# Optimization experiments

Measured on AMD Instinct MI355X. Metric: run time of the kernel, lower is better.

## Reference

```python
import jax, jax.numpy as jnp
import numpy as np


def gcn_conv(h, edge_index, num_nodes):
    # Symmetric-normalized GCN aggregation: out[i] = sum_{(j->i)} h[j] / sqrt(deg(i)*deg(j))
    row, col = edge_index[0], edge_index[1]
    deg = jax.ops.segment_sum(jnp.ones(col.shape, dtype=h.dtype), col, num_segments=num_nodes)
    d_inv_sqrt = jnp.where(deg > 0, jax.lax.rsqrt(jnp.maximum(deg, 1.0)), 0.0)
    w = d_inv_sqrt[row] * d_inv_sqrt[col]           # [E]
    msg = h[row] * w[:, None]                        # [E, D] gather + scale
    return jax.ops.segment_sum(msg, col, num_segments=num_nodes)  # [N, D] scatter-add


def setup_inputs() -> dict:
    key = jax.random.key(0)
    k1, k2, k3, k4 = jax.random.split(key, 4)
    N, E, F_IN, F_HID, F_OUT = 100000, 1600000, 128, 64, 40
    x = jax.random.normal(k1, (N, F_IN), dtype=jnp.float32)
    edge_index = jax.random.randint(k2, (2, E), 0, N, dtype=jnp.int64)
    # xavier_uniform with gain=1.414 (as in reset_parameters); biases zero
    def xavier(k, shape, gain=1.414):
        fan_out, fan_in = shape
        a = gain * np.sqrt(6.0 / (fan_in + fan_out))
        return jax.random.uniform(k, shape, jnp.float32, -a, a)
    W1 = xavier(k3, (F_HID, F_IN))
    b1 = jnp.zeros((F_HID,), dtype=jnp.float32)
    W2 = xavier(k4, (F_OUT, F_HID))
    b2 = jnp.zeros((F_OUT,), dtype=jnp.float32)
    return {"x": x, "edge_index": edge_index, "W1": W1, "b1": b1, "W2": W2, "b2": b2}


def reference(x, edge_index, W1, b1, W2, b2):
    # GNN.forward with num_layers=2, use_mp=True, eval mode (dropout inactive)
    N = x.shape[0]
    h = x @ W1.T                      # [N, nhid]
    h = gcn_conv(h, edge_index, N)
    h = jax.nn.relu(h + b1)
    h = h @ W2.T                      # [N, nclass]
    h = gcn_conv(h, edge_index, N)
    return h + b2
```

## Files before the change

### kernel.cpp

```cpp
#include <hip/hip_runtime.h>
#include <hip/hip_fp16.h>


typedef __attribute__((ext_vector_type(8))) _Float16 half8v;
typedef __attribute__((ext_vector_type(4))) float   float4v;

__global__ void k_detect(const int* __restrict__ ed, int* __restrict__ flag, int nwords) {
  __shared__ int any;
  if (threadIdx.x == 0) any = 0;
  __syncthreads();
  #pragma unroll
  for (int u = 0; u < 8; ++u) {
    int idx = 2 * (threadIdx.x * 8 + u) + 1;
    if (idx < nwords && ed[idx] != 0) any = 1;
  }
  __syncthreads();
  if (threadIdx.x == 0) *flag = any ? 0 : 1;
}

__global__ void k_binfill(const int* __restrict__ ed, const int* __restrict__ flag,
                          int* __restrict__ gbincnt, unsigned* __restrict__ binbuf,
                          int E, int cap) {
  __shared__ int hist[512];
  __shared__ int cursor[512];
  __shared__ unsigned rec[4096];
  __shared__ unsigned short binv[4096];
  int t = threadIdx.x;
  hist[t] = 0; hist[t + 256] = 0;
  __syncthreads();
  const int is64 = *flag;
  const int base = blockIdx.x * 4096;
  const int nE = min(4096, E - base);
  for (int j = t; j < nE; j += 256) {
    int e = base + j;
    int r = is64 ? ed[2 * e] : ed[e];
    int c = is64 ? ed[2 * (E + e)] : ed[E + e];
    rec[j] = (unsigned)r | ((unsigned)(c & 255) << 17);
    binv[j] = (unsigned short)(c >> 8);
    atomicAdd(&hist[c >> 8], 1);
  }
  __syncthreads();
  for (int b = t; b < 512; b += 256) {
    int h = hist[b];
    cursor[b] = h ? atomicAdd(&gbincnt[b], h) : 0;
  }
  __syncthreads();
  for (int j = t; j < nE; j += 256) {
    int bin = binv[j];
    int pos = atomicAdd(&cursor[bin], 1);
    if (pos < cap)
      binbuf[(size_t)bin * cap + pos] = rec[j];
  }
}

__global__ void k_binscan(const int* __restrict__ gbincnt, int* __restrict__ gbase,
                          int* __restrict__ rowptr, int NBINS, int N, int cap) {
  __shared__ int sd[512];
  int t = threadIdx.x;
  #pragma unroll
  for (int u = 0; u < 2; ++u) {
    int i = t + 256 * u;
    sd[i] = (i < NBINS) ? min(gbincnt[i], cap) : 0;
  }
  __syncthreads();
  for (int off = 1; off < 512; off <<= 1) {
    int v0 = (t >= off) ? sd[t - off] : 0;
    int i1 = t + 256;
    int v1 = sd[i1 - off];
    __syncthreads();
    sd[t] += v0; sd[i1] += v1;
    __syncthreads();
  }
  #pragma unroll
  for (int u = 0; u < 2; ++u) {
    int i = t + 256 * u;
    if (i < NBINS) gbase[i] = (i == 0) ? 0 : sd[i - 1];
  }
  if (t == 0) rowptr[N] = sd[NBINS - 1];
}

__global__ void k_degscat(const unsigned* __restrict__ binbuf, const int* __restrict__ gbincnt,
                          const int* __restrict__ gbase, float* __restrict__ dis,
                          int* __restrict__ rowptr, int* __restrict__ srcs, int N, int cap) {
  __shared__ int cnt[256];
  __shared__ int sd[256];
  __shared__ int cursor[256];
  __shared__ unsigned rec[8192];
  int t = threadIdx.x, b = blockIdx.x;
  cnt[t] = 0;
  __syncthreads();
  int n = min(gbincnt[b], cap);
  const unsigned* buf = binbuf + (size_t)b * cap;
  for (int j = t; j < n; j += 256) {
    unsigned v = buf[j];
    rec[j] = v;
    atomicAdd(&cnt[v >> 17], 1);
  }
  __syncthreads();
  sd[t] = cnt[t];
  __syncthreads();
  for (int off = 1; off < 256; off <<= 1) {
    int v = (t >= off) ? sd[t - off] : 0;
    __syncthreads();
    sd[t] += v;
    __syncthreads();
  }
  int rp = gbase[b] + ((t == 0) ? 0 : sd[t - 1]);
  cursor[t] = rp;
  int node = b * 256 + t;
  if (node < N) {
    int d = cnt[t];
    dis[node] = (d > 0) ? rsqrtf((float)d) : 0.f;
    rowptr[node] = rp;
  }
  __syncthreads();
  for (int j = t; j < n; j += 256) {
    unsigned v = rec[j];
    int pos = atomicAdd(&cursor[v >> 17], 1);
    srcs[pos] = (int)(v & 0x1FFFF);
  }
}

__launch_bounds__(256)
__global__ void k_gemm1_mfma(const float* __restrict__ X, const float* __restrict__ W,
                             const float* __restrict__ dis, __half* __restrict__ Y, int N) {
  __shared__ _Float16 xl[128 * 128];
  __shared__ _Float16 wl[64 * 128];
  const int t = threadIdx.x;
  const int row0 = blockIdx.x * 128;

  {
    int n = t >> 2, kb = (t & 3) * 32;
    const float* src = W + n * 128 + kb;
    #pragma unroll
    for (int j = 0; j < 4; ++j) {
      float4 va = *(const float4*)&src[j * 8];
      float4 vb = *(const float4*)&src[j * 8 + 4];
      _Float16 h8[8] = {(_Float16)va.x, (_Float16)va.y, (_Float16)va.z, (_Float16)va.w,
                        (_Float16)vb.x, (_Float16)vb.y, (_Float16)vb.z, (_Float16)vb.w};
      int k = kb + j * 8;
      *(float4*)&wl[n * 128 + (k ^ ((n & 7) * 8))] = *(float4*)h8;
    }
  }
  {
    int r = t >> 1, kb = (t & 1) * 64;
    int row = row0 + r;
    #pragma unroll
    for (int j = 0; j < 8; ++j) {
      float4 va = make_float4(0.f, 0.f, 0.f, 0.f), vb = va;
      if (row < N) {
        va = *(const float4*)&X[(size_t)row * 128 + kb + j * 8];
        vb = *(const float4*)&X[(size_t)row * 128 + kb + j * 8 + 4];
      }
      _Float16 h8[8] = {(_Float16)va.x, (_Float16)va.y, (_Float16)va.z, (_Float16)va.w,
                        (_Float16)vb.x, (_Float16)vb.y, (_Float16)vb.z, (_Float16)vb.w};
      int k = kb + j * 8;
      *(float4*)&xl[r * 128 + (k ^ ((r & 7) * 8))] = *(float4*)h8;
    }
  }
  __syncthreads();

  const int w = t >> 6, l = t & 63;
  const int m0 = w * 32;
  const int lr = l & 15, q = l >> 4;

  float4v acc[2][4] = {};
  #pragma unroll
  for (int kc = 0; kc < 4; ++kc) {
    half8v a[2], b[4];
    #pragma unroll
    for (int mt = 0; mt < 2; ++mt) {
      int m = m0 + mt * 16 + lr;
      int k = (kc * 32 + q * 8) ^ ((m & 7) * 8);
      a[mt] = *(half8v*)&xl[m * 128 + k];
    }
    #pragma unroll
    for (int nt = 0; nt < 4; ++nt) {
      int n = nt * 16 + lr;
      int k = (kc * 32 + q * 8) ^ ((n & 7) * 8);
      b[nt] = *(half8v*)&wl[n * 128 + k];
    }
    #pragma unroll
    for (int mt = 0; mt < 2; ++mt)
      #pragma unroll
      for (int nt = 0; nt < 4; ++nt)
        acc[mt][nt] = __builtin_amdgcn_mfma_f32_16x16x32_f16(a[mt], b[nt], acc[mt][nt], 0, 0, 0);
  }

  #pragma unroll
  for (int mt = 0; mt < 2; ++mt) {
    #pragma unroll
    for (int r = 0; r < 4; ++r) {
      int row = row0 + m0 + mt * 16 + q * 4 + r;
      if (row < N) {
        float dr = dis[row];
        #pragma unroll
        for (int nt = 0; nt < 4; ++nt)
          Y[(size_t)row * 64 + nt * 16 + lr] = __float2half_rn(acc[mt][nt][r] * dr);
      }
    }
  }
}

__launch_bounds__(256)
__global__ void k_gemm2_mfma(const __half* __restrict__ Xh, const float* __restrict__ W,
                             const float* __restrict__ dis, __half* __restrict__ Y, int N) {
  __shared__ _Float16 xl[128 * 64];
  __shared__ _Float16 wl[48 * 64];
  const int t = threadIdx.x;
  const int row0 = blockIdx.x * 128;

  for (int i = t; i < 48 * 8; i += 256) {
    int c = i >> 3, kq = i & 7;
    _Float16 h8[8];
    #pragma unroll
    for (int j = 0; j < 8; ++j)
      h8[j] = (c < 40) ? (_Float16)W[c * 64 + kq * 8 + j] : (_Float16)0.f;
    *(float4*)&wl[c * 64 + ((kq * 8) ^ ((c & 7) * 8))] = *(float4*)h8;
  }
  for (int i = t; i < 1024; i += 256) {
    int r = i >> 3, kq = i & 7;
    int row = row0 + r;
    float4 v = make_float4(0.f, 0.f, 0.f, 0.f);
    if (row < N) v = *(const float4*)&Xh[(size_t)row * 64 + kq * 8];
    *(float4*)&xl[r * 64 + ((kq * 8) ^ ((r & 7) * 8))] = v;
  }
  __syncthreads();

  const int w = t >> 6, l = t & 63;
  const int m0 = w * 32;
  const int lr = l & 15, q = l >> 4;

  float4v acc[2][3] = {};
  #pragma unroll
  for (int kc = 0; kc < 2; ++kc) {
    half8v a[2], b[3];
    #pragma unroll
    for (int mt = 0; mt < 2; ++mt) {
      int m = m0 + mt * 16 + lr;
      int k = (kc * 32 + q * 8) ^ ((m & 7) * 8);
      a[mt] = *(half8v*)&xl[m * 64 + k];
    }
    #pragma unroll
    for (int nt = 0; nt < 3; ++nt) {
      int n = nt * 16 + lr;
      int k = (kc * 32 + q * 8) ^ ((n & 7) * 8);
      b[nt] = *(half8v*)&wl[n * 64 + k];
    }
    #pragma unroll
    for (int mt = 0; mt < 2; ++mt)
      #pragma unroll
      for (int nt = 0; nt < 3; ++nt)
        acc[mt][nt] = __builtin_amdgcn_mfma_f32_16x16x32_f16(a[mt], b[nt], acc[mt][nt], 0, 0, 0);
  }

  #pragma unroll
  for (int mt = 0; mt < 2; ++mt) {
    #pragma unroll
    for (int r = 0; r < 4; ++r) {
      int row = row0 + m0 + mt * 16 + q * 4 + r;
      if (row < N) {
        float dr = dis[row];
        #pragma unroll
        for (int nt = 0; nt < 3; ++nt) {
          int col = nt * 16 + lr;
          if (col < 40)
            Y[(size_t)row * 40 + col] = __float2half_rn(acc[mt][nt][r] * dr);
        }
      }
    }
  }
}

__launch_bounds__(256)
__global__ void k_conv64(const __half* __restrict__ H, const int* __restrict__ rowptr,
                         const int* __restrict__ srcs, const float* __restrict__ dis,
                         const float* __restrict__ b1, __half* __restrict__ out, int N) {
  int node = blockIdx.x * 4 + (threadIdx.x >> 6);
  if (node >= N) return;
  int lane = threadIdx.x & 63;
  int g = lane >> 3, li = lane & 7;
  int s = rowptr[node], e = rowptr[node + 1];
  int last = e - 1;
  float a0 = 0.f, a1 = 0.f, a2 = 0.f, a3 = 0.f,
        a4 = 0.f, a5 = 0.f, a6 = 0.f, a7 = 0.f;
  for (int p = s; p < e; p += 32) {
    int sv = srcs[min(p + (lane & 31), last)];
    #pragma unroll
    for (int u = 0; u < 4; ++u) {
      int src = __shfl(sv, 8 * u + g);
      float4 raw = *(const float4*)&H[(size_t)src * 64 + 8 * li];
      if (p + 8 * u + g < e) {
        const __half2* hp = (const __half2*)&raw;
        float2 f0 = __half22float2(hp[0]);
        float2 f1 = __half22float2(hp[1]);
        float2 f2 = __half22float2(hp[2]);
        float2 f3 = __half22float2(hp[3]);
        a0 += f0.x; a1 += f0.y; a2 += f1.x; a3 += f1.y;
        a4 += f2.x; a5 += f2.y; a6 += f3.x; a7 += f3.y;
      }
    }
  }
  #pragma unroll
  for (int off = 8; off <= 32; off <<= 1) {
    a0 += __shfl_xor(a0, off); a1 += __shfl_xor(a1, off);
    a2 += __shfl_xor(a2, off); a3 += __shfl_xor(a3, off);
    a4 += __shfl_xor(a4, off); a5 += __shfl_xor(a5, off);
    a6 += __shfl_xor(a6, off); a7 += __shfl_xor(a7, off);
  }
  if (g == 0) {
    float dn = dis[node];
    const float* bb = b1 + 8 * li;
    __half hv[8];
    hv[0] = __float2half_rn(fmaxf(fmaf(a0, dn, bb[0]), 0.f));
    hv[1] = __float2half_rn(fmaxf(fmaf(a1, dn, bb[1]), 0.f));
    hv[2] = __float2half_rn(fmaxf(fmaf(a2, dn, bb[2]), 0.f));
    hv[3] = __float2half_rn(fmaxf(fmaf(a3, dn, bb[3]), 0.f));
    hv[4] = __float2half_rn(fmaxf(fmaf(a4, dn, bb[4]), 0.f));
    hv[5] = __float2half_rn(fmaxf(fmaf(a5, dn, bb[5]), 0.f));
    hv[6] = __float2half_rn(fmaxf(fmaf(a6, dn, bb[6]), 0.f));
    hv[7] = __float2half_rn(fmaxf(fmaf(a7, dn, bb[7]), 0.f));
    *(float4*)&out[(size_t)node * 64 + 8 * li] = *(float4*)hv;
  }
}

__launch_bounds__(256)
__global__ void k_conv40(const __half* __restrict__ H, const int* __restrict__ rowptr,
                         const int* __restrict__ srcs, const float* __restrict__ dis,
                         const float* __restrict__ b2, float* __restrict__ out, int N) {
  int node = blockIdx.x * 4 + (threadIdx.x >> 6);
  if (node >= N) return;
  int lane = threadIdx.x & 63;
  int g = lane >> 3, li = lane & 7;
  bool act = li < 5;
  int s = rowptr[node], e = rowptr[node + 1];
  int last = e - 1;
  float a0 = 0.f, a1 = 0.f, a2 = 0.f, a3 = 0.f,
        a4 = 0.f, a5 = 0.f, a6 = 0.f, a7 = 0.f;
  for (int p = s; p < e; p += 32) {
    int sv = srcs[min(p + (lane & 31), last)];
    #pragma unroll
    for (int u = 0; u < 4; ++u) {
      int src = __shfl(sv, 8 * u + g);
      if (act) {
        float4 raw = *(const float4*)&H[(size_t)src * 40 + 8 * li];
        if (p + 8 * u + g < e) {
          const __half2* hp = (const __half2*)&raw;
          float2 f0 = __half22float2(hp[0]);
          float2 f1 = __half22float2(hp[1]);
          float2 f2 = __half22float2(hp[2]);
          float2 f3 = __half22float2(hp[3]);
          a0 += f0.x; a1 += f0.y; a2 += f1.x; a3 += f1.y;
          a4 += f2.x; a5 += f2.y; a6 += f3.x; a7 += f3.y;
        }
      }
    }
  }
  #pragma unroll
  for (int off = 8; off <= 32; off <<= 1) {
    a0 += __shfl_xor(a0, off); a1 += __shfl_xor(a1, off);
    a2 += __shfl_xor(a2, off); a3 += __shfl_xor(a3, off);
    a4 += __shfl_xor(a4, off); a5 += __shfl_xor(a5, off);
    a6 += __shfl_xor(a6, off); a7 += __shfl_xor(a7, off);
  }
  if (g == 0 && act) {
    float dn = dis[node];
    const float* bb = b2 + 8 * li;
    float4 v0 = make_float4(fmaf(a0, dn, bb[0]), fmaf(a1, dn, bb[1]),
                            fmaf(a2, dn, bb[2]), fmaf(a3, dn, bb[3]));
    float4 v1 = make_float4(fmaf(a4, dn, bb[4]), fmaf(a5, dn, bb[5]),
                            fmaf(a6, dn, bb[6]), fmaf(a7, dn, bb[7]));
    *(float4*)&out[(size_t)node * 40 + 8 * li] = v0;
    *(float4*)&out[(size_t)node * 40 + 8 * li + 4] = v1;
  }
}

extern "C" void kernel_launch(void* const* d_in, const int* in_sizes, int n_in,
                              void* d_out, int out_size, void* d_ws, size_t ws_size,
                              hipStream_t stream) {
  const float* x  = (const float*)d_in[0];
  const int*   ed = (const int*)d_in[1];
  const float* W1 = (const float*)d_in[2];
  const float* b1 = (const float*)d_in[3];
  const float* W2 = (const float*)d_in[4];
  const float* b2 = (const float*)d_in[5];
  float* out = (float*)d_out;

  const int FIN = 128, FH = 64, FO = 40;
  const int N = in_sizes[0] / FIN;
  const int E = in_sizes[1] / 2;
  const int NBINS = (N + 255) >> 8;

  char* ws = (char*)d_ws;
  size_t off = 0;
  auto alloc = [&](size_t bytes) {
    void* p = ws + off;
    off = (off + bytes + 255) & ~(size_t)255;
    return p;
  };
  int*    flag    = (int*)alloc(4);
  int*    gbincnt = (int*)alloc(512 * 4);
  int*    gbase   = (int*)alloc(512 * 4);
  float*  dis     = (float*)alloc((size_t)N * 4);
  int*    rowptr  = (int*)alloc(((size_t)N + 1) * 4);
  int*    srcs    = (int*)alloc((size_t)E * 4);
  __half* h1      = (__half*)alloc((size_t)N * FH * 2);
  __half* h1b     = (__half*)alloc((size_t)N * FH * 2);
  __half* h2      = (__half*)alloc((size_t)N * FO * 2);
  int cap = (int)(((size_t)N * FH * 2) / ((size_t)NBINS * 4));
  if (cap > 8192) cap = 8192;
  unsigned* binbuf = (unsigned*)h1;

  hipMemsetAsync(gbincnt, 0, 512 * 4, stream);
  k_detect<<<1, 256, 0, stream>>>(ed, flag, in_sizes[1]);

  int fb = (E + 4095) / 4096;
  k_binfill<<<fb, 256, 0, stream>>>(ed, flag, gbincnt, binbuf, E, cap);
  k_binscan<<<1, 256, 0, stream>>>(gbincnt, gbase, rowptr, NBINS, N, cap);
  k_degscat<<<NBINS, 256, 0, stream>>>(binbuf, gbincnt, gbase, dis, rowptr, srcs, N, cap);

  int mb = (N + 127) / 128;
  int cb = (N + 3) / 4;
  k_gemm1_mfma<<<mb, 256, 0, stream>>>(x, W1, dis, h1, N);
  k_conv64<<<cb, 256, 0, stream>>>(h1, rowptr, srcs, dis, b1, h1b, N);
  k_gemm2_mfma<<<mb, 256, 0, stream>>>(h1b, W2, dis, h2, N);
  k_conv40<<<cb, 256, 0, stream>>>(h2, rowptr, srcs, dis, b2, out, N);
}
```

Baseline: 251.5 us.

## Quantize layer-2 features to int8, fold detect and scan kernels, recoalesce GEMM loads

Layer-2 features are now quantized to int8 with one fp32 scale per row, in 64-byte rows, so the second aggregation gathers fewer bytes per edge. The k_detect kernel is folded into every k_binfill block, and the k_binscan prefix scan is recomputed redundantly in every k_degscat block, which removes two launches. The gemm1 staging loads are reorganized so consecutive threads read consecutive float4s. The int8 quantization loses accuracy compared with fp16 and may fail tolerance checks.

```diff
diff --git a/kernel.cpp b/kernel.cpp
--- a/kernel.cpp
+++ b/kernel.cpp
@@ -5,30 +5,29 @@
 typedef __attribute__((ext_vector_type(8))) _Float16 half8v;
 typedef __attribute__((ext_vector_type(4))) float   float4v;
 
-__global__ void k_detect(const int* __restrict__ ed, int* __restrict__ flag, int nwords) {
-  __shared__ int any;
-  if (threadIdx.x == 0) any = 0;
-  __syncthreads();
-  #pragma unroll
-  for (int u = 0; u < 8; ++u) {
-    int idx = 2 * (threadIdx.x * 8 + u) + 1;
-    if (idx < nwords && ed[idx] != 0) any = 1;
-  }
-  __syncthreads();
-  if (threadIdx.x == 0) *flag = any ? 0 : 1;
-}
-
-__global__ void k_binfill(const int* __restrict__ ed, const int* __restrict__ flag,
+__global__ void k_binfill(const int* __restrict__ ed,
                           int* __restrict__ gbincnt, unsigned* __restrict__ binbuf,
                           int E, int cap) {
   __shared__ int hist[512];
   __shared__ int cursor[512];
   __shared__ unsigned rec[4096];
   __shared__ unsigned short binv[4096];
+  __shared__ int s_is64;
   int t = threadIdx.x;
   hist[t] = 0; hist[t + 256] = 0;
-  __syncthreads();
-  const int is64 = *flag;
+  if (t == 0) s_is64 = 1;
+  __syncthreads();
+  {
+    int any = 0;
+    #pragma unroll
+    for (int u = 0; u < 8; ++u) {
+      int idx = 2 * (t * 8 + u) + 1;
+      if (idx < 2 * E && ed[idx] != 0) any = 1;
+    }
+    if (any) s_is64 = 0;
+  }
+  __syncthreads();
+  const int is64 = s_is64;
   const int base = blockIdx.x * 4096;
   const int nE = min(4096, E - base);
   for (int j = t; j < nE; j += 256) {
@@ -53,42 +52,29 @@
   }
 }
 
-__global__ void k_binscan(const int* __restrict__ gbincnt, int* __restrict__ gbase,
-                          int* __restrict__ rowptr, int NBINS, int N, int cap) {
+__global__ void k_degscat(const unsigned* __restrict__ binbuf, const int* __restrict__ gbincnt,
+                          float* __restrict__ dis, int* __restrict__ rowptr,
+                          int* __restrict__ srcs, int NBINS, int N, int cap) {
   __shared__ int sd[512];
-  int t = threadIdx.x;
-  #pragma unroll
-  for (int u = 0; u < 2; ++u) {
-    int i = t + 256 * u;
-    sd[i] = (i < NBINS) ? min(gbincnt[i], cap) : 0;
-  }
-  __syncthreads();
-  for (int off = 1; off < 512; off <<= 1) {
-    int v0 = (t >= off) ? sd[t - off] : 0;
-    int i1 = t + 256;
-    int v1 = sd[i1 - off];
-    __syncthreads();
-    sd[t] += v0; sd[i1] += v1;
-    __syncthreads();
-  }
-  #pragma unroll
-  for (int u = 0; u < 2; ++u) {
-    int i = t + 256 * u;
-    if (i < NBINS) gbase[i] = (i == 0) ? 0 : sd[i - 1];
-  }
-  if (t == 0) rowptr[N] = sd[NBINS - 1];
-}
-
-__global__ void k_degscat(const unsigned* __restrict__ binbuf, const int* __restrict__ gbincnt,
-                          const int* __restrict__ gbase, float* __restrict__ dis,
-                          int* __restrict__ rowptr, int* __restrict__ srcs, int N, int cap) {
   __shared__ int cnt[256];
-  __shared__ int sd[256];
+  __shared__ int sc[256];
   __shared__ int cursor[256];
   __shared__ unsigned rec[8192];
   int t = threadIdx.x, b = blockIdx.x;
+  sd[t]       = (t < NBINS)       ? min(gbincnt[t], cap)       : 0;
+  sd[t + 256] = (t + 256 < NBINS) ? min(gbincnt[t + 256], cap) : 0;
   cnt[t] = 0;
   __syncthreads();
+  for (int off = 1; off < 512; off <<= 1) {
+    int v0 = (t >= off) ? sd[t - off] : 0;
+    int v1 = sd[t + 256 - off];
+    __syncthreads();
+    sd[t] += v0; sd[t + 256] += v1;
+    __syncthreads();
+  }
+  const int mybase = (b == 0) ? 0 : sd[b - 1];
+  if (b == NBINS - 1 && t == 0) rowptr[N] = sd[NBINS - 1];
+
   int n = min(gbincnt[b], cap);
   const unsigned* buf = binbuf + (size_t)b * cap;
   for (int j = t; j < n; j += 256) {
@@ -97,15 +83,15 @@
     atomicAdd(&cnt[v >> 17], 1);
   }
   __syncthreads();
-  sd[t] = cnt[t];
+  sc[t] = cnt[t];
   __syncthreads();
   for (int off = 1; off < 256; off <<= 1) {
-    int v = (t >= off) ? sd[t - off] : 0;
+    int v = (t >= off) ? sc[t - off] : 0;
     __syncthreads();
-    sd[t] += v;
+    sc[t] += v;
     __syncthreads();
   }
-  int rp = gbase[b] + ((t == 0) ? 0 : sd[t - 1]);
+  int rp = mybase + ((t == 0) ? 0 : sc[t - 1]);
   cursor[t] = rp;
   int node = b * 256 + t;
   if (node < N) {
@@ -129,34 +115,25 @@
   const int t = threadIdx.x;
   const int row0 = blockIdx.x * 128;
 
-  {
-    int n = t >> 2, kb = (t & 3) * 32;
-    const float* src = W + n * 128 + kb;
-    #pragma unroll
-    for (int j = 0; j < 4; ++j) {
-      float4 va = *(const float4*)&src[j * 8];
-      float4 vb = *(const float4*)&src[j * 8 + 4];
-      _Float16 h8[8] = {(_Float16)va.x, (_Float16)va.y, (_Float16)va.z, (_Float16)va.w,
-                        (_Float16)vb.x, (_Float16)vb.y, (_Float16)vb.z, (_Float16)vb.w};
-      int k = kb + j * 8;
-      *(float4*)&wl[n * 128 + (k ^ ((n & 7) * 8))] = *(float4*)h8;
-    }
-  }
-  {
-    int r = t >> 1, kb = (t & 1) * 64;
+  #pragma unroll
+  for (int j = 0; j < 8; ++j) {
+    int qq = t + 256 * j;
+    int r = qq >> 5, k4 = qq & 31;
+    float4 v = *(const float4*)&W[(size_t)r * 128 + k4 * 4];
+    _Float16 h4[4] = {(_Float16)v.x, (_Float16)v.y, (_Float16)v.z, (_Float16)v.w};
+    int k = (k4 * 4) ^ ((r & 7) * 8);
+    *(float2*)&wl[r * 128 + k] = *(float2*)h4;
+  }
+  #pragma unroll
+  for (int j = 0; j < 16; ++j) {
+    int qq = t + 256 * j;
+    int r = qq >> 5, k4 = qq & 31;
     int row = row0 + r;
-    #pragma unroll
-    for (int j = 0; j < 8; ++j) {
-      float4 va = make_float4(0.f, 0.f, 0.f, 0.f), vb = va;
-      if (row < N) {
-        va = *(const float4*)&X[(size_t)row * 128 + kb + j * 8];
-        vb = *(const float4*)&X[(size_t)row * 128 + kb + j * 8 + 4];
-      }
-      _Float16 h8[8] = {(_Float16)va.x, (_Float16)va.y, (_Float16)va.z, (_Float16)va.w,
-                        (_Float16)vb.x, (_Float16)vb.y, (_Float16)vb.z, (_Float16)vb.w};
-      int k = kb + j * 8;
-      *(float4*)&xl[r * 128 + (k ^ ((r & 7) * 8))] = *(float4*)h8;
-    }
+    float4 v = make_float4(0.f, 0.f, 0.f, 0.f);
+    if (row < N) v = *(const float4*)&X[(size_t)row * 128 + k4 * 4];
+    _Float16 h4[4] = {(_Float16)v.x, (_Float16)v.y, (_Float16)v.z, (_Float16)v.w};
+    int k = (k4 * 4) ^ ((r & 7) * 8);
+    *(float2*)&xl[r * 128 + k] = *(float2*)h4;
   }
   __syncthreads();
 
@@ -204,7 +181,8 @@
 
 __launch_bounds__(256)
 __global__ void k_gemm2_mfma(const __half* __restrict__ Xh, const float* __restrict__ W,
-                             const float* __restrict__ dis, __half* __restrict__ Y, int N) {
+                             const float* __restrict__ dis, unsigned char* __restrict__ h2,
+                             int N) {
   __shared__ _Float16 xl[128 * 64];
   __shared__ _Float16 wl[48 * 64];
   const int t = threadIdx.x;
@@ -261,12 +239,27 @@
       int row = row0 + m0 + mt * 16 + q * 4 + r;
       if (row < N) {
         float dr = dis[row];
+        float v0 = acc[mt][0][r] * dr;
+        float v1 = acc[mt][1][r] * dr;
+        float v2 = acc[mt][2][r] * dr;
+        float m = fmaxf(fabsf(v0), fmaxf(fabsf(v1), fabsf(v2)));
         #pragma unroll
-        for (int nt = 0; nt < 3; ++nt) {
-          int col = nt * 16 + lr;
-          if (col < 40)
-            Y[(size_t)row * 40 + col] = __float2half_rn(acc[mt][nt][r] * dr);
-        }
+        for (int off = 1; off < 16; off <<= 1)
+          m = fmaxf(m, __shfl_xor(m, off));
+        float s = m * (1.f / 127.f);
+        float inv = (m > 0.f) ? (127.f / m) : 0.f;
+        unsigned char* dst = h2 + (size_t)row * 64;
+        int q0 = (int)rintf(v0 * inv);
+        int q1 = (int)rintf(v1 * inv);
+        int q2 = (int)rintf(v2 * inv);
+        q0 = max(-127, min(127, q0));
+        q1 = max(-127, min(127, q1));
+        q2 = max(-127, min(127, q2));
+        dst[lr]      = (unsigned char)(signed char)q0;
+        dst[lr + 16] = (unsigned char)(signed char)q1;
+        if (lr + 32 < 40) dst[lr + 32] = (unsigned char)(signed char)q2;
+        if (lr == 0) *(float*)&dst[40] = s;
+        if (lr >= 1 && lr <= 5) *(int*)&dst[40 + 4 * lr] = 0;
       }
     }
   }
@@ -325,7 +318,7 @@
 }
 
 __launch_bounds__(256)
-__global__ void k_conv40(const __half* __restrict__ H, const int* __restrict__ rowptr,
+__global__ void k_conv40(const unsigned char* __restrict__ H, const int* __restrict__ rowptr,
                          const int* __restrict__ srcs, const float* __restrict__ dis,
                          const float* __restrict__ b2, float* __restrict__ out, int N) {
   int node = blockIdx.x * 4 + (threadIdx.x >> 6);
@@ -343,15 +336,19 @@
     for (int u = 0; u < 4; ++u) {
       int src = __shfl(sv, 8 * u + g);
       if (act) {
-        float4 raw = *(const float4*)&H[(size_t)src * 40 + 8 * li];
+        const unsigned char* rowp = &H[(size_t)src * 64];
+        uint2 raw = *(const uint2*)&rowp[8 * li];
+        float sc = *(const float*)&rowp[40];
         if (p + 8 * u + g < e) {
-          const __half2* hp = (const __half2*)&raw;
-          float2 f0 = __half22float2(hp[0]);
-          float2 f1 = __half22float2(hp[1]);
-          float2 f2 = __half22float2(hp[2]);
-          float2 f3 = __half22float2(hp[3]);
-          a0 += f0.x; a1 += f0.y; a2 += f1.x; a3 += f1.y;
-          a4 += f2.x; a5 += f2.y; a6 += f3.x; a7 += f3.y;
+          int x0 = (int)raw.x, x1 = (int)raw.y;
+          a0 = fmaf((float)((x0 << 24) >> 24), sc, a0);
+          a1 = fmaf((float)((x0 << 16) >> 24), sc, a1);
+          a2 = fmaf((float)((x0 << 8)  >> 24), sc, a2);
+          a3 = fmaf((float)( x0        >> 24), sc, a3);
+          a4 = fmaf((float)((x1 << 24) >> 24), sc, a4);
+          a5 = fmaf((float)((x1 << 16) >> 24), sc, a5);
+          a6 = fmaf((float)((x1 << 8)  >> 24), sc, a6);
+          a7 = fmaf((float)( x1        >> 24), sc, a7);
         }
       }
     }
@@ -386,7 +383,7 @@
   const float* b2 = (const float*)d_in[5];
   float* out = (float*)d_out;
 
-  const int FIN = 128, FH = 64, FO = 40;
+  const int FIN = 128, FH = 64;
   const int N = in_sizes[0] / FIN;
   const int E = in_sizes[1] / 2;
   const int NBINS = (N + 255) >> 8;
@@ -398,26 +395,22 @@
     off = (off + bytes + 255) & ~(size_t)255;
     return p;
   };
-  int*    flag    = (int*)alloc(4);
-  int*    gbincnt = (int*)alloc(512 * 4);
-  int*    gbase   = (int*)alloc(512 * 4);
-  float*  dis     = (float*)alloc((size_t)N * 4);
-  int*    rowptr  = (int*)alloc(((size_t)N + 1) * 4);
-  int*    srcs    = (int*)alloc((size_t)E * 4);
-  __half* h1      = (__half*)alloc((size_t)N * FH * 2);
-  __half* h1b     = (__half*)alloc((size_t)N * FH * 2);
-  __half* h2      = (__half*)alloc((size_t)N * FO * 2);
+  int*           gbincnt = (int*)alloc(512 * 4);
+  float*         dis     = (float*)alloc((size_t)N * 4);
+  int*           rowptr  = (int*)alloc(((size_t)N + 1) * 4);
+  int*           srcs    = (int*)alloc((size_t)E * 4);
+  __half*        h1      = (__half*)alloc((size_t)N * FH * 2);
+  __half*        h1b     = (__half*)alloc((size_t)N * FH * 2);
+  unsigned char* h2      = (unsigned char*)alloc((size_t)N * 64);
   int cap = (int)(((size_t)N * FH * 2) / ((size_t)NBINS * 4));
   if (cap > 8192) cap = 8192;
   unsigned* binbuf = (unsigned*)h1;
 
   hipMemsetAsync(gbincnt, 0, 512 * 4, stream);
-  k_detect<<<1, 256, 0, stream>>>(ed, flag, in_sizes[1]);
 
   int fb = (E + 4095) / 4096;
-  k_binfill<<<fb, 256, 0, stream>>>(ed, flag, gbincnt, binbuf, E, cap);
-  k_binscan<<<1, 256, 0, stream>>>(gbincnt, gbase, rowptr, NBINS, N, cap);
-  k_degscat<<<NBINS, 256, 0, stream>>>(binbuf, gbincnt, gbase, dis, rowptr, srcs, N, cap);
+  k_binfill<<<fb, 256, 0, stream>>>(ed, gbincnt, binbuf, E, cap);
+  k_degscat<<<NBINS, 256, 0, stream>>>(binbuf, gbincnt, dis, rowptr, srcs, NBINS, N, cap);
 
   int mb = (N + 127) / 128;
   int cb = (N + 3) / 4;
```

New measurement: 246.8 us. No clear change (-1.9%).
